# Kernel optimization log

Measured on AMD Instinct MI355X. Metric: run time of the kernel, lower is better.

The kernel has to match this reference:

```python
import jax, jax.numpy as jnp
import numpy as np

P_K = 3  # patch kernel size
MV_SCALE = 32.0  # flow scale from STN: u/w*2*32


def unfold3(x):
    # torch.nn.Unfold(kernel_size=3, padding=1, stride=1), channel-major ordering
    B, C, H, W = x.shape
    xp = jnp.pad(x, ((0, 0), (0, 0), (1, 1), (1, 1)))
    # index = c*9 + i*3 + j, matching torch Unfold layout
    patches = jnp.stack([xp[:, :, i:i + H, j:j + W]
                         for i in range(P_K) for j in range(P_K)], axis=2)
    return patches  # [B, C, 9, H, W]


def bilinear_sample(img, gx, gy):
    # grid_sample, mode=bilinear, padding_mode=border, align_corners=True
    # img: [B, Cp, H, W]; gx, gy: [B, H, W] in [-1, 1]
    B, Cp, H, W = img.shape
    x = (gx + 1.0) * 0.5 * (W - 1)
    y = (gy + 1.0) * 0.5 * (H - 1)
    x0 = jnp.floor(x)
    y0 = jnp.floor(y)
    wx = (x - x0)[:, None]  # [B,1,H,W]
    wy = (y - y0)[:, None]
    x0i = jnp.clip(x0.astype(jnp.int32), 0, W - 1)
    x1i = jnp.clip(x0i + 1, 0, W - 1)
    y0i = jnp.clip(y0.astype(jnp.int32), 0, H - 1)
    y1i = jnp.clip(y0i + 1, 0, H - 1)
    imgf = img.reshape(B, Cp, H * W)

    def gather(yi, xi):
        idx = (yi * W + xi).reshape(B, -1)  # [B, H*W]
        out = jax.vmap(lambda im, ix: im[:, ix])(imgf, idx)
        return out.reshape(B, Cp, H, W)

    v00 = gather(y0i, x0i)
    v01 = gather(y0i, x1i)
    v10 = gather(y1i, x0i)
    v11 = gather(y1i, x1i)
    return (v00 * (1 - wx) * (1 - wy) + v01 * wx * (1 - wy)
            + v10 * (1 - wx) * wy + v11 * wx * wy)


def setup_inputs() -> dict:
    key = jax.random.key(0)
    ks = jax.random.split(key, 8)
    B, C, H, W = 4, 64, 128, 128
    nf = 64
    cin = nf * P_K * P_K * 2  # 1152
    inp = {
        'nbh_fea': jax.random.normal(ks[0], (B, C, H, W), jnp.float32),
        'cen_fea': jax.random.normal(ks[1], (B, C, H, W), jnp.float32),
        'mv': jax.random.normal(ks[2], (B, 2, H, W), jnp.float32),
        'w1': jax.random.normal(ks[3], (nf, cin), jnp.float32) * 0.02,
        'b1': jnp.zeros((nf,), jnp.float32),
        'w2': jax.random.normal(ks[4], (P_K * P_K, nf), jnp.float32) * 0.05,
        'b2': jnp.zeros((P_K * P_K,), jnp.float32),
    }
    return inp


def reference(nbh_fea, cen_fea, mv, w1, b1, w2, b2):
    B, C, H, W = cen_fea.shape
    K2 = P_K * P_K
    nbh_p = unfold3(nbh_fea).reshape(B, C * K2, H, W)
    cen_p = unfold3(cen_fea).reshape(B, C * K2, H, W)
    # identity mesh in [-1,1], xy indexing (x along W, y along H)
    xv, yv = jnp.meshgrid(jnp.linspace(-1.0, 1.0, W), jnp.linspace(-1.0, 1.0, H))
    u = mv[:, 0] / W * 2.0 * MV_SCALE
    v = mv[:, 1] / H * 2.0 * MV_SCALE
    gx = jnp.clip(xv[None] + u, -1.0, 1.0)
    gy = jnp.clip(yv[None] + v, -1.0, 1.0)
    aligned = bilinear_sample(nbh_p, gx, gy)  # [B, C*9, H, W]
    fuse = jnp.concatenate([aligned, cen_p], axis=1)  # [B, 2*C*9, H, W]
    h1 = jnp.einsum('bchw,oc->bohw', fuse, w1) + b1[None, :, None, None]
    h1 = jnp.where(h1 >= 0, h1, 0.1 * h1)  # LeakyReLU(0.1)
    h2 = jnp.einsum('bchw,oc->bohw', h1, w2) + b2[None, :, None, None]
    attn = jax.nn.softmax(h2, axis=1)  # [B, 9, H, W]
    out = jnp.mean(aligned.reshape(B, C, K2, H, W) * attn[:, None], axis=2)
    return out  # [B, C, H, W]
```

## Files before the change

kernel.cpp:

```cpp
#include <hip/hip_runtime.h>

#define B_   4
#define H_   128
#define W_   128
#define HW_  (H_*W_)
#define CIN_ 1152

typedef __attribute__((ext_vector_type(8))) short short8;
typedef __attribute__((ext_vector_type(4))) float floatx4;
typedef unsigned short u16;
typedef unsigned int   u32;

__device__ __forceinline__ float bf2f(u16 u){ union{u32 i; float f;} v; v.i=((u32)u)<<16; return v.f; }
__device__ __forceinline__ u16 f2bf(float f){ union{float fl; u32 i;} v; v.fl=f; u32 lsb=(v.i>>16)&1u; v.i += 0x7fffu + lsb; return (u16)(v.i>>16); }

__global__ void k_prep_w(const float* __restrict__ w1,
                         u16* __restrict__ WtA, u16* __restrict__ WtB){
    int o = blockIdx.x, sel = blockIdx.y, k = threadIdx.x;
    int c = k & 63, ij = k >> 6;
    float v = w1[(long)o*CIN_ + sel*576 + c*9 + ij];
    u16* dst = sel ? WtB : WtA;
    dst[o*576 + ij*64 + c] = f2bf(v);
}

__global__ __launch_bounds__(256) void k_t_fwd(
        const float* __restrict__ nbh, const float* __restrict__ cen,
        u16* __restrict__ nbhT, u16* __restrict__ cenT){
    __shared__ u16 tile[64*68];
    int px0 = blockIdx.x * 64;
    int b   = blockIdx.y;
    const float* src = blockIdx.z ? cen : nbh;
    u16* dst         = blockIdx.z ? cenT : nbhT;
    int t  = threadIdx.x;
    int hi = t >> 4, seg = t & 15;
    #pragma unroll
    for (int p = 0; p < 4; ++p){
        int c = p*16 + hi;
        float4 v = *reinterpret_cast<const float4*>(&src[(size_t)(b*64 + c)*HW_ + px0 + seg*4]);
        u16 pk[4] = { f2bf(v.x), f2bf(v.y), f2bf(v.z), f2bf(v.w) };
        *reinterpret_cast<uint2*>(&tile[c*68 + seg*4]) = *reinterpret_cast<uint2*>(pk);
    }
    __syncthreads();
    #pragma unroll
    for (int p = 0; p < 4; ++p){
        int px = p*16 + hi;
        int cg = seg*4;
        u16 pk[4] = { tile[cg*68+px], tile[(cg+1)*68+px], tile[(cg+2)*68+px], tile[(cg+3)*68+px] };
        *reinterpret_cast<uint2*>(&dst[(size_t)(b*HW_ + px0 + px)*64 + cg]) = *reinterpret_cast<uint2*>(pk);
    }
}

__global__ __launch_bounds__(256) void k_conv(
        const u16* __restrict__ nbhT, const u16* __restrict__ cenT,
        const u16* __restrict__ WtA, const u16* __restrict__ WtB,
        u16* __restrict__ convA, u16* __restrict__ convB){
    __shared__ __align__(16) u16 wtile[2][64*72];
    int x0  = blockIdx.x * 64;
    int y0  = blockIdx.y * 4;
    int b   = blockIdx.z >> 1;
    int sel = blockIdx.z & 1;
    const u16* src = sel ? cenT : nbhT;
    const u16* wt  = sel ? WtB : WtA;
    u16* dst       = sel ? convB : convA;
    int tid  = threadIdx.x;
    int lane = tid & 63, m = lane & 15, qd = lane >> 4, w = tid >> 6;
    int gy   = y0 + w;

    for (int q = tid; q < 64*8; q += 256){
        int o = q >> 3, c8 = q & 7;
        *reinterpret_cast<uint4*>(&wtile[0][o*72 + c8*8]) =
            *reinterpret_cast<const uint4*>(&wt[o*576 + c8*8]);
    }

    const size_t rowstride = (size_t)W_*64;
    const u16* img = src + (size_t)b*HW_*64;
    floatx4 acc[4][4] = {};

    #pragma unroll
    for (int ij = 0; ij < 9; ++ij){
        __syncthreads();
        if (ij < 8){
            int nij = ij + 1;
            for (int q = tid; q < 64*8; q += 256){
                int o = q >> 3, c8 = q & 7;
                *reinterpret_cast<uint4*>(&wtile[nij & 1][o*72 + c8*8]) =
                    *reinterpret_cast<const uint4*>(&wt[o*576 + nij*64 + c8*8]);
            }
        }
        const int i = ij/3, j = ij%3;
        int ry = gy + i - 1;
        if (ry >= 0 && ry < H_){
            const u16* srow = img + (size_t)ry*rowstride;
            #pragma unroll
            for (int s = 0; s < 2; ++s){
                int c0 = s*32 + qd*8;
                short8 bv[4];
                #pragma unroll
                for (int nt = 0; nt < 4; ++nt)
                    bv[nt] = *reinterpret_cast<const short8*>(&wtile[ij & 1][(nt*16 + m)*72 + c0]);
                #pragma unroll
                for (int mt = 0; mt < 4; ++mt){
                    int gx = x0 - 1 + mt*16 + m + j;
                    short8 av = {0,0,0,0,0,0,0,0};
                    if (gx >= 0 && gx < W_)
                        av = *reinterpret_cast<const short8*>(&srow[(size_t)gx*64 + c0]);
                    #pragma unroll
                    for (int nt = 0; nt < 4; ++nt)
                        acc[mt][nt] = __builtin_amdgcn_mfma_f32_16x16x32_bf16(av, bv[nt], acc[mt][nt], 0, 0, 0);
                }
            }
        }
    }

    size_t base = ((size_t)(b*HW_ + gy*W_ + x0))*64;
    #pragma unroll
    for (int mt = 0; mt < 4; ++mt)
        #pragma unroll
        for (int nt = 0; nt < 4; ++nt)
            #pragma unroll
            for (int r = 0; r < 4; ++r){
                int px = mt*16 + qd*4 + r;
                int o  = nt*16 + m;
                dst[base + (size_t)px*64 + o] = f2bf(acc[mt][nt][r]);
            }
}

__device__ __forceinline__ float fetchA(float am, int lane, int i, int j){
    bool ok = (i >= 1) & (i <= 3) & (j >= 1) & (j <= 3);
    int k = (i-1)*3 + (j-1);
    k = min(max(k, 0), 8);
    float v = __shfl(am, (lane & 48) | k, 64);
    return ok ? v : 0.f;
}

__global__ __launch_bounds__(512) void k_attn(
        const u16* __restrict__ nbhT,
        const u16* __restrict__ convA, const u16* __restrict__ convB,
        const float* __restrict__ mv,
        const float* __restrict__ b1, const float* __restrict__ w2,
        const float* __restrict__ b2, float* __restrict__ out){
    __shared__ __align__(16) int cwoff[64*16*2];
    __shared__ float otile[64*66];
    int tid  = threadIdx.x;
    int lane = tid & 63;
    int w    = tid >> 6;
    int m    = lane & 15;
    int qd   = lane >> 4;
    int pix0 = blockIdx.x*64;
    int b    = pix0 >> 14;
    int y    = (pix0 >> 7) & 127;
    int xblk = pix0 & 127;
    size_t pb = (size_t)b*HW_*64;
    const u16* nb = nbhT + pb;

    if (w < 4){
        int x = xblk + w*16 + m;
        float u  = mv[(long)(b*2  )*HW_ + y*W_ + x] * 0.5f;
        float v  = mv[(long)(b*2+1)*HW_ + y*W_ + x] * 0.5f;
        float gx = fminf(fmaxf(-1.0f + x*(2.0f/127.0f) + u, -1.f), 1.f);
        float gy = fminf(fmaxf(-1.0f + y*(2.0f/127.0f) + v, -1.f), 1.f);
        float sx = (gx + 1.f) * 63.5f;
        float sy = (gy + 1.f) * 63.5f;
        float x0f = floorf(sx), y0f = floorf(sy);
        float wx = sx - x0f,    wy = sy - y0f;
        int x0i = min(max((int)x0f, 0), W_-1);
        int y0i = min(max((int)y0f, 0), H_-1);
        int x1i = min(x0i+1, W_-1);
        int y1i = min(y0i+1, H_-1);
        float wx0 = 1.f - wx, wy0 = 1.f - wy;

        short8 av[2];
        #pragma unroll
        for (int s = 0; s < 2; ++s){
            int c0 = s*32 + qd*8;
            short8 q00 = *reinterpret_cast<const short8*>(&convA[pb + (size_t)(y0i*W_+x0i)*64 + c0]);
            short8 q01 = *reinterpret_cast<const short8*>(&convA[pb + (size_t)(y0i*W_+x1i)*64 + c0]);
            short8 q10 = *reinterpret_cast<const short8*>(&convA[pb + (size_t)(y1i*W_+x0i)*64 + c0]);
            short8 q11 = *reinterpret_cast<const short8*>(&convA[pb + (size_t)(y1i*W_+x1i)*64 + c0]);
            short8 qc  = *reinterpret_cast<const short8*>(&convB[pb + (size_t)(y*W_+x)*64 + c0]);
            short8 h;
            #pragma unroll
            for (int j = 0; j < 8; ++j){
                float t = wy0*(wx0*bf2f((u16)q00[j]) + wx*bf2f((u16)q01[j]))
                        + wy *(wx0*bf2f((u16)q10[j]) + wx*bf2f((u16)q11[j]))
                        + bf2f((u16)qc[j]) + b1[c0+j];
                t = t >= 0.f ? t : 0.1f*t;
                h[j] = (short)f2bf(t);
            }
            av[s] = h;
        }
        short8 bv[2];
        #pragma unroll
        for (int s = 0; s < 2; ++s){
            int c0 = s*32 + qd*8;
            short8 t = {0,0,0,0,0,0,0,0};
            if (m < 9){
                #pragma unroll
                for (int j = 0; j < 8; ++j) t[j] = (short)f2bf(w2[m*64 + c0 + j]);
            }
            bv[s] = t;
        }
        floatx4 C = {0.f,0.f,0.f,0.f};
        C = __builtin_amdgcn_mfma_f32_16x16x32_bf16(av[0], bv[0], C, 0, 0, 0);
        C = __builtin_amdgcn_mfma_f32_16x16x32_bf16(av[1], bv[1], C, 0, 0, 0);

        float b2k = (m < 9) ? b2[m] : 0.f;
        float am[4];
        #pragma unroll
        for (int r = 0; r < 4; ++r){
            float e  = C[r] + b2k;
            float mx = (m < 9) ? e : -3.0e38f;
            #pragma unroll
            for (int d = 1; d < 16; d <<= 1) mx = fmaxf(mx, __shfl_xor(mx, d, 64));
            float a = (m < 9) ? __expf(e - mx) : 0.f;
            float s = a;
            #pragma unroll
            for (int d = 1; d < 16; d <<= 1) s += __shfl_xor(s, d, 64);
            am[r] = a / (9.f * s);
        }

        int gpack = x0i | (y0i << 8) | ((y1i > y0i) ? 0x10000 : 0) | ((x1i > x0i) ? 0x20000 : 0);
        int at = m >> 2, bt = m & 3;
        #pragma unroll
        for (int r = 0; r < 4; ++r){
            int p   = qd*4 + r;
            int src = (lane & 48) | p;
            float wxp = __shfl(wx, src, 64);
            float wyp = __shfl(wy, src, 64);
            int   gp  = __shfl(gpack, src, 64);
            int x0p = gp & 255, y0p = (gp >> 8) & 255;
            int dy1 = (gp >> 16) & 1, dx1 = (gp >> 17) & 1;
            float wx0p = 1.f - wxp, wy0p = 1.f - wyp;
            int ia = dy1 ? at : at+1;
            int jb = dx1 ? bt : bt+1;
            float cw = wy0p*wx0p*fetchA(am[r], lane, at+1, bt+1)
                     + wy0p*wxp *fetchA(am[r], lane, at+1, jb)
                     + wyp *wx0p*fetchA(am[r], lane, ia,   bt+1)
                     + wyp *wxp *fetchA(am[r], lane, ia,   jb);
            int ry = y0p - 1 + at, rx = x0p - 1 + bt;
            bool ok = (ry >= 0) & (ry < H_) & (rx >= 0) & (rx < W_);
            int2 pr;
            pr.x = __float_as_int(ok ? cw : 0.f);
            pr.y = ok ? (ry*W_ + rx)*64 : 0;
            *reinterpret_cast<int2*>(&cwoff[((w*16 + p)*16 + m)*2]) = pr;
        }
    }
    __syncthreads();

    const u16* nbl = nb + lane;
    #pragma unroll
    for (int sp = 0; sp < 8; sp += 2){
        int slot0 = w*8 + sp;
        const int4* a4 = reinterpret_cast<const int4*>(&cwoff[slot0*32]);
        const int4* b4 = reinterpret_cast<const int4*>(&cwoff[(slot0+1)*32]);
        float acc0 = 0.f, acc1 = 0.f;
        #pragma unroll
        for (int k = 0; k < 8; ++k){
            int4 pa = a4[k];
            int4 pbv = b4[k];
            acc0 += __int_as_float(pa.x)  * bf2f(nbl[(size_t)pa.y]);
            acc1 += __int_as_float(pbv.x) * bf2f(nbl[(size_t)pbv.y]);
            acc0 += __int_as_float(pa.z)  * bf2f(nbl[(size_t)pa.w]);
            acc1 += __int_as_float(pbv.z) * bf2f(nbl[(size_t)pbv.w]);
        }
        otile[lane*66 + slot0]     = acc0;
        otile[lane*66 + slot0 + 1] = acc1;
    }
    __syncthreads();

    int px = lane;
    #pragma unroll
    for (int p = 0; p < 8; ++p){
        int c = w*8 + p;
        out[(size_t)(b*64 + c)*HW_ + y*W_ + xblk + px] = otile[c*66 + px];
    }
}

extern "C" void kernel_launch(void* const* d_in, const int* in_sizes, int n_in,
                              void* d_out, int out_size, void* d_ws, size_t ws_size,
                              hipStream_t stream){
    const float* nbh = (const float*)d_in[0];
    const float* cen = (const float*)d_in[1];
    const float* mv  = (const float*)d_in[2];
    const float* w1  = (const float*)d_in[3];
    const float* b1  = (const float*)d_in[4];
    const float* w2  = (const float*)d_in[5];
    const float* b2  = (const float*)d_in[6];
    float* out = (float*)d_out;

    const size_t IMG = (size_t)B_*HW_*64;
    char* ws = (char*)d_ws;
    u16* WtA   = (u16*)ws;
    u16* WtB   = WtA + 64*576;
    u16* convA = (u16*)(ws + 147456);
    u16* convB = convA + IMG;
    u16* nbhT  = convB + IMG;
    u16* cenT  = nbhT  + IMG;

    hipLaunchKernelGGL(k_prep_w, dim3(64,2),    dim3(576), 0, stream, w1, WtA, WtB);
    hipLaunchKernelGGL(k_t_fwd,  dim3(256,4,2), dim3(256), 0, stream, nbh, cen, nbhT, cenT);
    hipLaunchKernelGGL(k_conv,   dim3(2,32,8),  dim3(256), 0, stream,
                       nbhT, cenT, WtA, WtB, convA, convB);
    hipLaunchKernelGGL(k_attn,   dim3(1024),    dim3(512), 0, stream,
                       nbhT, convA, convB, mv, b1, w2, b2, out);
}
```

Measured before the change: 144.5 us.

## Fold weight prep into transpose kernel, precast w2, and pair-channel gather in attn

Merges the w1 bf16 repack kernel into the transpose kernel as an extra grid slice, which removes one launch. That slice also converts w2 to bf16 once, so k_attn loads short8 directly instead of converting per lane. b1 is now read with float4 loads. The final gather is restructured: each lane loads two adjacent channels as one u32, and the two wave halves split the 16 taps and combine through a shuffle. otile is padded to 67 to avoid LDS bank conflicts, at the cost of extra shuffles and half-idle stores.

```diff
diff --git a/kernel.cpp b/kernel.cpp
--- a/kernel.cpp
+++ b/kernel.cpp
@@ -14,24 +14,35 @@
 __device__ __forceinline__ float bf2f(u16 u){ union{u32 i; float f;} v; v.i=((u32)u)<<16; return v.f; }
 __device__ __forceinline__ u16 f2bf(float f){ union{float fl; u32 i;} v; v.fl=f; u32 lsb=(v.i>>16)&1u; v.i += 0x7fffu + lsb; return (u16)(v.i>>16); }
 
-__global__ void k_prep_w(const float* __restrict__ w1,
-                         u16* __restrict__ WtA, u16* __restrict__ WtB){
-    int o = blockIdx.x, sel = blockIdx.y, k = threadIdx.x;
-    int c = k & 63, ij = k >> 6;
-    float v = w1[(long)o*CIN_ + sel*576 + c*9 + ij];
-    u16* dst = sel ? WtB : WtA;
-    dst[o*576 + ij*64 + c] = f2bf(v);
-}
-
 __global__ __launch_bounds__(256) void k_t_fwd(
         const float* __restrict__ nbh, const float* __restrict__ cen,
-        u16* __restrict__ nbhT, u16* __restrict__ cenT){
+        const float* __restrict__ w1, const float* __restrict__ w2,
+        u16* __restrict__ nbhT, u16* __restrict__ cenT,
+        u16* __restrict__ WtA, u16* __restrict__ WtB, u16* __restrict__ w2bf){
     __shared__ u16 tile[64*68];
+    int t = threadIdx.x;
+    if (blockIdx.z == 2){
+        int id = blockIdx.y*256 + blockIdx.x;
+        if (id < 288){
+            int e = id*256 + t;
+            int o = e / 1152;
+            int r = e - o*1152;
+            int sel = r / 576;
+            int k = r - sel*576;
+            int c = k & 63, ij = k >> 6;
+            float v = w1[(long)o*CIN_ + sel*576 + c*9 + ij];
+            u16* dst = sel ? WtB : WtA;
+            dst[o*576 + ij*64 + c] = f2bf(v);
+        } else if (id == 288){
+            for (int e = t; e < 576; e += 256)
+                w2bf[e] = f2bf(w2[e]);
+        }
+        return;
+    }
     int px0 = blockIdx.x * 64;
     int b   = blockIdx.y;
     const float* src = blockIdx.z ? cen : nbh;
     u16* dst         = blockIdx.z ? cenT : nbhT;
-    int t  = threadIdx.x;
     int hi = t >> 4, seg = t & 15;
     #pragma unroll
     for (int p = 0; p < 4; ++p){
@@ -137,10 +148,10 @@
         const u16* __restrict__ nbhT,
         const u16* __restrict__ convA, const u16* __restrict__ convB,
         const float* __restrict__ mv,
-        const float* __restrict__ b1, const float* __restrict__ w2,
+        const float* __restrict__ b1, const u16* __restrict__ w2bf,
         const float* __restrict__ b2, float* __restrict__ out){
     __shared__ __align__(16) int cwoff[64*16*2];
-    __shared__ float otile[64*66];
+    __shared__ float otile[64*67];
     int tid  = threadIdx.x;
     int lane = tid & 63;
     int w    = tid >> 6;
@@ -178,12 +189,15 @@
             short8 q10 = *reinterpret_cast<const short8*>(&convA[pb + (size_t)(y1i*W_+x0i)*64 + c0]);
             short8 q11 = *reinterpret_cast<const short8*>(&convA[pb + (size_t)(y1i*W_+x1i)*64 + c0]);
             short8 qc  = *reinterpret_cast<const short8*>(&convB[pb + (size_t)(y*W_+x)*64 + c0]);
+            float b1l[8];
+            *reinterpret_cast<float4*>(&b1l[0]) = *reinterpret_cast<const float4*>(&b1[c0]);
+            *reinterpret_cast<float4*>(&b1l[4]) = *reinterpret_cast<const float4*>(&b1[c0+4]);
             short8 h;
             #pragma unroll
             for (int j = 0; j < 8; ++j){
                 float t = wy0*(wx0*bf2f((u16)q00[j]) + wx*bf2f((u16)q01[j]))
                         + wy *(wx0*bf2f((u16)q10[j]) + wx*bf2f((u16)q11[j]))
-                        + bf2f((u16)qc[j]) + b1[c0+j];
+                        + bf2f((u16)qc[j]) + b1l[j];
                 t = t >= 0.f ? t : 0.1f*t;
                 h[j] = (short)f2bf(t);
             }
@@ -192,12 +206,9 @@
         short8 bv[2];
         #pragma unroll
         for (int s = 0; s < 2; ++s){
-            int c0 = s*32 + qd*8;
             short8 t = {0,0,0,0,0,0,0,0};
-            if (m < 9){
-                #pragma unroll
-                for (int j = 0; j < 8; ++j) t[j] = (short)f2bf(w2[m*64 + c0 + j]);
-            }
+            if (m < 9)
+                t = *reinterpret_cast<const short8*>(&w2bf[m*64 + s*32 + qd*8]);
             bv[s] = t;
         }
         floatx4 C = {0.f,0.f,0.f,0.f};
@@ -247,24 +258,39 @@
     }
     __syncthreads();
 
-    const u16* nbl = nb + lane;
+    int half = lane >> 5;
+    int cp   = lane & 31;
+    const u16* nbl = nb + 2*cp;
+    const int2* ctab = reinterpret_cast<const int2*>(cwoff);
     #pragma unroll
     for (int sp = 0; sp < 8; sp += 2){
-        int slot0 = w*8 + sp;
-        const int4* a4 = reinterpret_cast<const int4*>(&cwoff[slot0*32]);
-        const int4* b4 = reinterpret_cast<const int4*>(&cwoff[(slot0+1)*32]);
-        float acc0 = 0.f, acc1 = 0.f;
+        int s0 = w*8 + sp, s1 = s0 + 1;
+        const int2* t0 = ctab + s0*16;
+        const int2* t1 = ctab + s1*16;
+        float a0 = 0.f, a1 = 0.f, c0a = 0.f, c1a = 0.f;
         #pragma unroll
         for (int k = 0; k < 8; ++k){
-            int4 pa = a4[k];
-            int4 pbv = b4[k];
-            acc0 += __int_as_float(pa.x)  * bf2f(nbl[(size_t)pa.y]);
-            acc1 += __int_as_float(pbv.x) * bf2f(nbl[(size_t)pbv.y]);
-            acc0 += __int_as_float(pa.z)  * bf2f(nbl[(size_t)pa.w]);
-            acc1 += __int_as_float(pbv.z) * bf2f(nbl[(size_t)pbv.w]);
-        }
-        otile[lane*66 + slot0]     = acc0;
-        otile[lane*66 + slot0 + 1] = acc1;
+            int2 p0 = t0[2*k + half];
+            int2 p1 = t1[2*k + half];
+            u32 v0 = *reinterpret_cast<const u32*>(&nbl[(size_t)p0.y]);
+            u32 v1 = *reinterpret_cast<const u32*>(&nbl[(size_t)p1.y]);
+            float cw0 = __int_as_float(p0.x), cw1 = __int_as_float(p1.x);
+            a0  += cw0 * bf2f((u16)(v0 & 0xffffu));
+            a1  += cw0 * bf2f((u16)(v0 >> 16));
+            c0a += cw1 * bf2f((u16)(v1 & 0xffffu));
+            c1a += cw1 * bf2f((u16)(v1 >> 16));
+        }
+        a0  += __shfl_xor(a0, 32, 64);
+        a1  += __shfl_xor(a1, 32, 64);
+        c0a += __shfl_xor(c0a, 32, 64);
+        c1a += __shfl_xor(c1a, 32, 64);
+        if (half == 0){
+            int c2 = 2*cp;
+            otile[c2*67 + s0]     = a0;
+            otile[(c2+1)*67 + s0] = a1;
+            otile[c2*67 + s1]     = c0a;
+            otile[(c2+1)*67 + s1] = c1a;
+        }
     }
     __syncthreads();
 
@@ -272,7 +298,7 @@
     #pragma unroll
     for (int p = 0; p < 8; ++p){
         int c = w*8 + p;
-        out[(size_t)(b*64 + c)*HW_ + y*W_ + xblk + px] = otile[c*66 + px];
+        out[(size_t)(b*64 + c)*HW_ + y*W_ + xblk + px] = otile[c*67 + px];
     }
 }
 
@@ -292,15 +318,16 @@
     char* ws = (char*)d_ws;
     u16* WtA   = (u16*)ws;
     u16* WtB   = WtA + 64*576;
-    u16* convA = (u16*)(ws + 147456);
+    u16* w2bf  = (u16*)(ws + 147456);
+    u16* convA = (u16*)(ws + 151552);
     u16* convB = convA + IMG;
     u16* nbhT  = convB + IMG;
     u16* cenT  = nbhT  + IMG;
 
-    hipLaunchKernelGGL(k_prep_w, dim3(64,2),    dim3(576), 0, stream, w1, WtA, WtB);
-    hipLaunchKernelGGL(k_t_fwd,  dim3(256,4,2), dim3(256), 0, stream, nbh, cen, nbhT, cenT);
-    hipLaunchKernelGGL(k_conv,   dim3(2,32,8),  dim3(256), 0, stream,
+    hipLaunchKernelGGL(k_t_fwd, dim3(256,4,3), dim3(256), 0, stream,
+                       nbh, cen, w1, w2, nbhT, cenT, WtA, WtB, w2bf);
+    hipLaunchKernelGGL(k_conv,  dim3(2,32,8),  dim3(256), 0, stream,
                        nbhT, cenT, WtA, WtB, convA, convB);
-    hipLaunchKernelGGL(k_attn,   dim3(1024),    dim3(512), 0, stream,
-                       nbhT, convA, convB, mv, b1, w2, b2, out);
-}
+    hipLaunchKernelGGL(k_attn,  dim3(1024),    dim3(512), 0, stream,
+                       nbhT, convA, convB, mv, b1, w2bf, b2, out);
+}
```

After: 140.3 us. -2.9%, faster.
